# Kernel tuning notes

Measured on AMD Instinct MI355X. Metric: run time of the kernel, lower is better.

Reference implementation:

```python
import jax, jax.numpy as jnp
import numpy as np

OBS, ACT, LAT, H = 64, 32, 25, 5
B = 8192
SUP_H = 64


def setup_inputs() -> dict:
    key = jax.random.key(0)
    ks = jax.random.split(key, 12)
    s = 0.1
    inp = {
        'obs': jax.random.normal(ks[0], (B, OBS), jnp.float32),
        # supervisor FeedForward: OBS -> 64 -> 64 -> LAT, ReLU hidden, Sigmoid output
        'sw1': jax.random.normal(ks[1], (OBS, SUP_H), jnp.float32) * s,
        'sb1': jnp.zeros((SUP_H,), jnp.float32),
        'sw2': jax.random.normal(ks[2], (SUP_H, SUP_H), jnp.float32) * s,
        'sb2': jnp.zeros((SUP_H,), jnp.float32),
        'sw3': jax.random.normal(ks[3], (SUP_H, LAT), jnp.float32) * s,
        'sb3': jnp.zeros((LAT,), jnp.float32),
        # OBS*ACT tiny reflex FeedForwards 1 -> H -> 1, stacked into batched params
        'rw1': jax.random.normal(ks[4], (OBS, ACT, H), jnp.float32) * s,
        'rb1': jnp.zeros((OBS, ACT, H), jnp.float32),
        'rw2': jax.random.normal(ks[5], (OBS, ACT, H), jnp.float32) * s,
        'rb2': jnp.zeros((OBS, ACT), jnp.float32),
        # activation matrix (LAT, OBS, ACT)
        'act_matrix': jnp.ones((LAT, OBS, ACT), jnp.float32),
    }
    return inp


def reference(obs, sw1, sb1, sw2, sb2, sw3, sb3, rw1, rb1, rw2, rb2, act_matrix):
    # supervisor: (B, LAT) sigmoid latent activations
    h = jax.nn.relu(obs @ sw1 + sb1)
    h = jax.nn.relu(h @ sw2 + sb2)
    latent = jax.nn.sigmoid(h @ sw3 + sb3)

    # reflex gating: (B, LAT) x (LAT, OBS, ACT) -> (B, OBS, ACT), softmax over ACT
    logits = jnp.einsum('bl,loa->boa', latent, act_matrix)
    reflex_acts = jax.nn.softmax(logits, axis=-1)

    # all OBS*ACT tiny 1->H->1 MLPs, batched: input is obs[:, o] (scalar per net)
    # hidden: (B, OBS, ACT, H)
    rh = jax.nn.relu(obs[:, :, None, None] * rw1[None] + rb1[None])
    reflex_out = jnp.einsum('boah,oah->boa', rh, rw2) + rb2[None]  # (B, OBS, ACT)

    # weighted sum over obs dim -> (B, ACT)
    return jnp.sum(reflex_out * reflex_acts, axis=1)
```

## Files before the change

kernel.cpp:

```cpp
#include <hip/hip_runtime.h>


#define TOBS 64
#define TACT 32
#define TLAT 25
#define TB   8192
#define BT   16
#define NCH  16
#define HSTR 68

#define DPP_ADD(x, ctrl) \
  ((x) + __builtin_bit_cast(float, __builtin_amdgcn_update_dpp( \
      0, __builtin_bit_cast(int, (x)), (ctrl), 0xF, 0xF, true)))

__device__ __forceinline__ float halfwave_sum(float x) {
    x = DPP_ADD(x, 0xB1);
    x = DPP_ADD(x, 0x4E);
    x = DPP_ADD(x, 0x141);
    x = DPP_ADD(x, 0x140);
    int y = __builtin_amdgcn_ds_swizzle(__builtin_bit_cast(int, x), 0x401F);
    return x + __builtin_bit_cast(float, y);
}

__device__ __forceinline__ float sigmoidf_(float x) {
    return 1.0f / (1.0f + __expf(-x));
}

__global__ __launch_bounds__(256, 2)
void reflex_fused(const float* __restrict__ obs,
                  const float* __restrict__ sw1, const float* __restrict__ sb1,
                  const float* __restrict__ sw2, const float* __restrict__ sb2,
                  const float* __restrict__ sw3, const float* __restrict__ sb3,
                  const float* __restrict__ rw1, const float* __restrict__ rb1,
                  const float* __restrict__ rw2, const float* __restrict__ rb2,
                  const float* __restrict__ am,  float* __restrict__ out)
{
    __shared__ __align__(16) float obs_s[BT * HSTR];
    __shared__ __align__(16) float lat_s[BT * 26];
    __shared__ __align__(16) union {
        struct { float h1[BT * HSTR]; float h2[BT * HSTR]; } p1;
        struct { float4 At4[2][25 * 32]; float4 W4[2][16 * 32]; } p2;
    } U;

    const int tid  = threadIdx.x;
    const int row0 = blockIdx.x * BT;

    {
        const int r = tid >> 4, f = tid & 15;
        *(float4*)&obs_s[r * HSTR + f * 4] =
            *(const float4*)&obs[(row0 + r) * TOBS + f * 4];
    }
    __syncthreads();

    {
        const int r = tid >> 4, j0 = (tid & 15) * 4;
        float4 acc = *(const float4*)&sb1[j0];
        #pragma unroll 8
        for (int k = 0; k < 64; ++k) {
            float x = obs_s[r * HSTR + k];
            const float4 w = *(const float4*)&sw1[k * 64 + j0];
            acc.x = fmaf(x, w.x, acc.x); acc.y = fmaf(x, w.y, acc.y);
            acc.z = fmaf(x, w.z, acc.z); acc.w = fmaf(x, w.w, acc.w);
        }
        *(float4*)&U.p1.h1[r * HSTR + j0] =
            make_float4(fmaxf(acc.x, 0.f), fmaxf(acc.y, 0.f),
                        fmaxf(acc.z, 0.f), fmaxf(acc.w, 0.f));
    }
    __syncthreads();

    {
        const int r = tid >> 4, j0 = (tid & 15) * 4;
        float4 acc = *(const float4*)&sb2[j0];
        #pragma unroll 8
        for (int k = 0; k < 64; ++k) {
            float x = U.p1.h1[r * HSTR + k];
            const float4 w = *(const float4*)&sw2[k * 64 + j0];
            acc.x = fmaf(x, w.x, acc.x); acc.y = fmaf(x, w.y, acc.y);
            acc.z = fmaf(x, w.z, acc.z); acc.w = fmaf(x, w.w, acc.w);
        }
        *(float4*)&U.p1.h2[r * HSTR + j0] =
            make_float4(fmaxf(acc.x, 0.f), fmaxf(acc.y, 0.f),
                        fmaxf(acc.z, 0.f), fmaxf(acc.w, 0.f));
    }
    __syncthreads();

    {
        const int r = tid >> 4, q = tid & 15;
        if (q < 13) {
            const int j = q * 2;
            float a0 = sb3[j];
            float a1 = (j + 1 < TLAT) ? sb3[j + 1] : 0.f;
            #pragma unroll 8
            for (int k = 0; k < 64; ++k) {
                float x = U.p1.h2[r * HSTR + k];
                a0 = fmaf(x, sw3[k * TLAT + j], a0);
                if (j + 1 < TLAT) a1 = fmaf(x, sw3[k * TLAT + j + 1], a1);
            }
            lat_s[r * 26 + j] = sigmoidf_(a0);
            if (j + 1 < TLAT) lat_s[r * 26 + j + 1] = sigmoidf_(a1);
        }
    }
    __syncthreads();

    const int a  = tid & 31;
    const int hw = tid >> 5;
    const int r0 = hw * 2, r1 = r0 + 1;

    float latA[TLAT], latB[TLAT];
    #pragma unroll
    for (int l = 0; l < TLAT; ++l) {
        latA[l] = lat_s[r0 * 26 + l];
        latB[l] = lat_s[r1 * 26 + l];
    }

    auto wload = [&](int k, int n) -> float {
        if (k < 5)  return rw1[n * 5 + k];
        if (k < 10) return rb1[n * 5 + (k - 5)];
        if (k < 15) return rw2[n * 5 + (k - 10)];
        return rb2[n];
    };

    auto stage = [&](int c, int b) {
        const int cb = c * 128;
        {
            int e = tid, l = e >> 5, a_ = e & 31;
            const float* g = am + l * 2048 + cb + a_;
            float4 v; v.x = g[0]; v.y = g[32]; v.z = g[64]; v.w = g[96];
            U.p2.At4[b][e] = v;

            e = tid + 256; l = e >> 5; a_ = e & 31;
            const float* g2 = am + l * 2048 + cb + a_;
            float4 v2; v2.x = g2[0]; v2.y = g2[32]; v2.z = g2[64]; v2.w = g2[96];
            U.p2.At4[b][e] = v2;

            e = tid + 512; l = e >> 5; a_ = e & 31;
            const float* g3 = am + l * 2048 + cb + a_;
            float4 v3; v3.x = g3[0]; v3.y = g3[32]; v3.z = g3[64]; v3.w = g3[96];
            U.p2.At4[b][e] = v3;

            if (tid < 32) {
                e = tid + 768;
                const float* g4 = am + 24 * 2048 + cb + tid;
                float4 v4; v4.x = g4[0]; v4.y = g4[32]; v4.z = g4[64]; v4.w = g4[96];
                U.p2.At4[b][e] = v4;
            }
        }
        {
            int k = tid >> 5, a_ = tid & 31;
            int n0 = cb + a_;
            float4 w;
            w.x = wload(k, n0);      w.y = wload(k, n0 + 32);
            w.z = wload(k, n0 + 64); w.w = wload(k, n0 + 96);
            U.p2.W4[b][tid] = w;

            k += 8;
            float4 w2;
            w2.x = wload(k, n0);      w2.y = wload(k, n0 + 32);
            w2.z = wload(k, n0 + 64); w2.w = wload(k, n0 + 96);
            U.p2.W4[b][tid + 256] = w2;
        }
    };

    float acc0 = 0.f, acc1 = 0.f;

    stage(0, 0);
    __syncthreads();

    for (int c = 0; c < NCH; ++c) {
        const float4* A4 = U.p2.At4[c & 1];
        const float4* Wb = U.p2.W4[c & 1];

        float l00 = 0.f, l01 = 0.f, l02 = 0.f, l03 = 0.f;
        float l10 = 0.f, l11 = 0.f, l12 = 0.f, l13 = 0.f;
        #pragma unroll
        for (int l = 0; l < TLAT; ++l) {
            const float4 q = A4[l * 32 + a];
            l00 = fmaf(q.x, latA[l], l00); l10 = fmaf(q.x, latB[l], l10);
            l01 = fmaf(q.y, latA[l], l01); l11 = fmaf(q.y, latB[l], l11);
            l02 = fmaf(q.z, latA[l], l02); l12 = fmaf(q.z, latB[l], l12);
            l03 = fmaf(q.w, latA[l], l03); l13 = fmaf(q.w, latB[l], l13);
        }

        float e00 = __expf(l00), e01 = __expf(l01), e02 = __expf(l02), e03 = __expf(l03);
        float e10 = __expf(l10), e11 = __expf(l11), e12 = __expf(l12), e13 = __expf(l13);
        float p00 = e00 * __builtin_amdgcn_rcpf(halfwave_sum(e00));
        float p01 = e01 * __builtin_amdgcn_rcpf(halfwave_sum(e01));
        float p02 = e02 * __builtin_amdgcn_rcpf(halfwave_sum(e02));
        float p03 = e03 * __builtin_amdgcn_rcpf(halfwave_sum(e03));
        float p10 = e10 * __builtin_amdgcn_rcpf(halfwave_sum(e10));
        float p11 = e11 * __builtin_amdgcn_rcpf(halfwave_sum(e11));
        float p12 = e12 * __builtin_amdgcn_rcpf(halfwave_sum(e12));
        float p13 = e13 * __builtin_amdgcn_rcpf(halfwave_sum(e13));

        const int ob = c * 4;
        const float x00 = obs_s[r0 * HSTR + ob],     x10 = obs_s[r1 * HSTR + ob];
        const float x01 = obs_s[r0 * HSTR + ob + 1], x11 = obs_s[r1 * HSTR + ob + 1];
        const float x02 = obs_s[r0 * HSTR + ob + 2], x12 = obs_s[r1 * HSTR + ob + 2];
        const float x03 = obs_s[r0 * HSTR + ob + 3], x13 = obs_s[r1 * HSTR + ob + 3];

        const float4 B2 = Wb[15 * 32 + a];
        float q00 = B2.x, q01 = B2.y, q02 = B2.z, q03 = B2.w;
        float q10 = B2.x, q11 = B2.y, q12 = B2.z, q13 = B2.w;
        #pragma unroll
        for (int h = 0; h < 5; ++h) {
            const float4 w1v = Wb[h * 32 + a];
            const float4 b1v = Wb[(5 + h) * 32 + a];
            const float4 w2v = Wb[(10 + h) * 32 + a];
            q00 = fmaf(fmaxf(fmaf(x00, w1v.x, b1v.x), 0.f), w2v.x, q00);
            q10 = fmaf(fmaxf(fmaf(x10, w1v.x, b1v.x), 0.f), w2v.x, q10);
            q01 = fmaf(fmaxf(fmaf(x01, w1v.y, b1v.y), 0.f), w2v.y, q01);
            q11 = fmaf(fmaxf(fmaf(x11, w1v.y, b1v.y), 0.f), w2v.y, q11);
            q02 = fmaf(fmaxf(fmaf(x02, w1v.z, b1v.z), 0.f), w2v.z, q02);
            q12 = fmaf(fmaxf(fmaf(x12, w1v.z, b1v.z), 0.f), w2v.z, q12);
            q03 = fmaf(fmaxf(fmaf(x03, w1v.w, b1v.w), 0.f), w2v.w, q03);
            q13 = fmaf(fmaxf(fmaf(x13, w1v.w, b1v.w), 0.f), w2v.w, q13);
        }

        acc0 = fmaf(q00, p00, acc0); acc1 = fmaf(q10, p10, acc1);
        acc0 = fmaf(q01, p01, acc0); acc1 = fmaf(q11, p11, acc1);
        acc0 = fmaf(q02, p02, acc0); acc1 = fmaf(q12, p12, acc1);
        acc0 = fmaf(q03, p03, acc0); acc1 = fmaf(q13, p13, acc1);

        if (c + 1 < NCH) stage(c + 1, (c + 1) & 1);
        __syncthreads();
    }

    out[(row0 + r0) * TACT + a] = acc0;
    out[(row0 + r1) * TACT + a] = acc1;
}

extern "C" void kernel_launch(void* const* d_in, const int* in_sizes, int n_in,
                              void* d_out, int out_size, void* d_ws, size_t ws_size,
                              hipStream_t stream) {
    const float* obs = (const float*)d_in[0];
    const float* sw1 = (const float*)d_in[1];
    const float* sb1 = (const float*)d_in[2];
    const float* sw2 = (const float*)d_in[3];
    const float* sb2 = (const float*)d_in[4];
    const float* sw3 = (const float*)d_in[5];
    const float* sb3 = (const float*)d_in[6];
    const float* rw1 = (const float*)d_in[7];
    const float* rb1 = (const float*)d_in[8];
    const float* rw2 = (const float*)d_in[9];
    const float* rb2 = (const float*)d_in[10];
    const float* am  = (const float*)d_in[11];
    float* out = (float*)d_out;

    reflex_fused<<<TB / BT, 256, 0, stream>>>(obs, sw1, sb1, sw2, sb2, sw3, sb3,
                                              rw1, rb1, rw2, rb2, am, out);
}
```

Baseline: 57.97 us.

## Split obs dimension across block pairs and widen per-thread row tile to four

```diff
diff --git a/kernel.cpp b/kernel.cpp
--- a/kernel.cpp
+++ b/kernel.cpp
@@ -5,8 +5,8 @@
 #define TACT 32
 #define TLAT 25
 #define TB   8192
-#define BT   16
-#define NCH  16
+#define BT   32
+#define NCH  8
 #define HSTR 68
 
 #define DPP_ADD(x, ctrl) \
@@ -26,7 +26,7 @@
     return 1.0f / (1.0f + __expf(-x));
 }
 
-__global__ __launch_bounds__(256, 2)
+__global__ __launch_bounds__(256, 1)
 void reflex_fused(const float* __restrict__ obs,
                   const float* __restrict__ sw1, const float* __restrict__ sb1,
                   const float* __restrict__ sw2, const float* __restrict__ sb2,
@@ -42,76 +42,92 @@
         struct { float4 At4[2][25 * 32]; float4 W4[2][16 * 32]; } p2;
     } U;
 
-    const int tid  = threadIdx.x;
-    const int row0 = blockIdx.x * BT;
-
-    {
-        const int r = tid >> 4, f = tid & 15;
-        *(float4*)&obs_s[r * HSTR + f * 4] =
-            *(const float4*)&obs[(row0 + r) * TOBS + f * 4];
-    }
-    __syncthreads();
-
-    {
-        const int r = tid >> 4, j0 = (tid & 15) * 4;
-        float4 acc = *(const float4*)&sb1[j0];
-        #pragma unroll 8
-        for (int k = 0; k < 64; ++k) {
-            float x = obs_s[r * HSTR + k];
-            const float4 w = *(const float4*)&sw1[k * 64 + j0];
-            acc.x = fmaf(x, w.x, acc.x); acc.y = fmaf(x, w.y, acc.y);
-            acc.z = fmaf(x, w.z, acc.z); acc.w = fmaf(x, w.w, acc.w);
-        }
-        *(float4*)&U.p1.h1[r * HSTR + j0] =
-            make_float4(fmaxf(acc.x, 0.f), fmaxf(acc.y, 0.f),
-                        fmaxf(acc.z, 0.f), fmaxf(acc.w, 0.f));
-    }
-    __syncthreads();
-
-    {
-        const int r = tid >> 4, j0 = (tid & 15) * 4;
-        float4 acc = *(const float4*)&sb2[j0];
-        #pragma unroll 8
-        for (int k = 0; k < 64; ++k) {
-            float x = U.p1.h1[r * HSTR + k];
-            const float4 w = *(const float4*)&sw2[k * 64 + j0];
-            acc.x = fmaf(x, w.x, acc.x); acc.y = fmaf(x, w.y, acc.y);
-            acc.z = fmaf(x, w.z, acc.z); acc.w = fmaf(x, w.w, acc.w);
-        }
-        *(float4*)&U.p1.h2[r * HSTR + j0] =
-            make_float4(fmaxf(acc.x, 0.f), fmaxf(acc.y, 0.f),
-                        fmaxf(acc.z, 0.f), fmaxf(acc.w, 0.f));
-    }
-    __syncthreads();
-
-    {
-        const int r = tid >> 4, q = tid & 15;
+    const int tid   = threadIdx.x;
+    const int bid   = blockIdx.x;
+    const int row0  = (bid >> 1) * BT;
+    const int obase = (bid & 1) * 32;
+
+    {
+        const int r = tid >> 3, f = tid & 7;
+        *(float4*)&obs_s[r * HSTR + f * 8] =
+            *(const float4*)&obs[(row0 + r) * TOBS + f * 8];
+        *(float4*)&obs_s[r * HSTR + f * 8 + 4] =
+            *(const float4*)&obs[(row0 + r) * TOBS + f * 8 + 4];
+    }
+    __syncthreads();
+
+    {
+        const int rr = tid >> 4, j0 = (tid & 15) * 4;
+        #pragma unroll
+        for (int rp = 0; rp < BT; rp += 16) {
+            const int r = rp + rr;
+            float4 acc = *(const float4*)&sb1[j0];
+            #pragma unroll 8
+            for (int k = 0; k < 64; ++k) {
+                float x = obs_s[r * HSTR + k];
+                const float4 w = *(const float4*)&sw1[k * 64 + j0];
+                acc.x = fmaf(x, w.x, acc.x); acc.y = fmaf(x, w.y, acc.y);
+                acc.z = fmaf(x, w.z, acc.z); acc.w = fmaf(x, w.w, acc.w);
+            }
+            *(float4*)&U.p1.h1[r * HSTR + j0] =
+                make_float4(fmaxf(acc.x, 0.f), fmaxf(acc.y, 0.f),
+                            fmaxf(acc.z, 0.f), fmaxf(acc.w, 0.f));
+        }
+    }
+    __syncthreads();
+
+    {
+        const int rr = tid >> 4, j0 = (tid & 15) * 4;
+        #pragma unroll
+        for (int rp = 0; rp < BT; rp += 16) {
+            const int r = rp + rr;
+            float4 acc = *(const float4*)&sb2[j0];
+            #pragma unroll 8
+            for (int k = 0; k < 64; ++k) {
+                float x = U.p1.h1[r * HSTR + k];
+                const float4 w = *(const float4*)&sw2[k * 64 + j0];
+                acc.x = fmaf(x, w.x, acc.x); acc.y = fmaf(x, w.y, acc.y);
+                acc.z = fmaf(x, w.z, acc.z); acc.w = fmaf(x, w.w, acc.w);
+            }
+            *(float4*)&U.p1.h2[r * HSTR + j0] =
+                make_float4(fmaxf(acc.x, 0.f), fmaxf(acc.y, 0.f),
+                            fmaxf(acc.z, 0.f), fmaxf(acc.w, 0.f));
+        }
+    }
+    __syncthreads();
+
+    {
+        const int rr = tid >> 4, q = tid & 15;
         if (q < 13) {
             const int j = q * 2;
-            float a0 = sb3[j];
-            float a1 = (j + 1 < TLAT) ? sb3[j + 1] : 0.f;
-            #pragma unroll 8
-            for (int k = 0; k < 64; ++k) {
-                float x = U.p1.h2[r * HSTR + k];
-                a0 = fmaf(x, sw3[k * TLAT + j], a0);
-                if (j + 1 < TLAT) a1 = fmaf(x, sw3[k * TLAT + j + 1], a1);
-            }
-            lat_s[r * 26 + j] = sigmoidf_(a0);
-            if (j + 1 < TLAT) lat_s[r * 26 + j + 1] = sigmoidf_(a1);
+            #pragma unroll
+            for (int rp = 0; rp < BT; rp += 16) {
+                const int r = rp + rr;
+                float a0 = sb3[j];
+                float a1 = (j + 1 < TLAT) ? sb3[j + 1] : 0.f;
+                #pragma unroll 8
+                for (int k = 0; k < 64; ++k) {
+                    float x = U.p1.h2[r * HSTR + k];
+                    a0 = fmaf(x, sw3[k * TLAT + j], a0);
+                    if (j + 1 < TLAT) a1 = fmaf(x, sw3[k * TLAT + j + 1], a1);
+                }
+                lat_s[r * 26 + j] = sigmoidf_(a0);
+                if (j + 1 < TLAT) lat_s[r * 26 + j + 1] = sigmoidf_(a1);
+            }
         }
     }
     __syncthreads();
 
     const int a  = tid & 31;
-    const int hw = tid >> 5;
-    const int r0 = hw * 2, r1 = r0 + 1;
-
-    float latA[TLAT], latB[TLAT];
+    const int g  = tid >> 5;
+    const int r0 = g * 4;
+
+    float lat[4][25];
     #pragma unroll
-    for (int l = 0; l < TLAT; ++l) {
-        latA[l] = lat_s[r0 * 26 + l];
-        latB[l] = lat_s[r1 * 26 + l];
-    }
+    for (int rr = 0; rr < 4; ++rr)
+        #pragma unroll
+        for (int l = 0; l < TLAT; ++l)
+            lat[rr][l] = lat_s[(r0 + rr) * 26 + l];
 
     auto wload = [&](int k, int n) -> float {
         if (k < 5)  return rw1[n * 5 + k];
@@ -121,11 +137,11 @@
     };
 
     auto stage = [&](int c, int b) {
-        const int cb = c * 128;
+        const int cb = obase * 32 + c * 128;
         {
             int e = tid, l = e >> 5, a_ = e & 31;
-            const float* g = am + l * 2048 + cb + a_;
-            float4 v; v.x = g[0]; v.y = g[32]; v.z = g[64]; v.w = g[96];
+            const float* gp = am + l * 2048 + cb + a_;
+            float4 v; v.x = gp[0]; v.y = gp[32]; v.z = gp[64]; v.w = gp[96];
             U.p2.At4[b][e] = v;
 
             e = tid + 256; l = e >> 5; a_ = e & 31;
@@ -139,10 +155,9 @@
             U.p2.At4[b][e] = v3;
 
             if (tid < 32) {
-                e = tid + 768;
                 const float* g4 = am + 24 * 2048 + cb + tid;
                 float4 v4; v4.x = g4[0]; v4.y = g4[32]; v4.z = g4[64]; v4.w = g4[96];
-                U.p2.At4[b][e] = v4;
+                U.p2.At4[b][tid + 768] = v4;
             }
         }
         {
@@ -161,7 +176,7 @@
         }
     };
 
-    float acc0 = 0.f, acc1 = 0.f;
+    float acc[4] = {0.f, 0.f, 0.f, 0.f};
 
     stage(0, 0);
     __syncthreads();
@@ -170,63 +185,80 @@
         const float4* A4 = U.p2.At4[c & 1];
         const float4* Wb = U.p2.W4[c & 1];
 
-        float l00 = 0.f, l01 = 0.f, l02 = 0.f, l03 = 0.f;
-        float l10 = 0.f, l11 = 0.f, l12 = 0.f, l13 = 0.f;
+        float lg[4][4] = {{0.f,0.f,0.f,0.f},{0.f,0.f,0.f,0.f},
+                          {0.f,0.f,0.f,0.f},{0.f,0.f,0.f,0.f}};
         #pragma unroll
         for (int l = 0; l < TLAT; ++l) {
             const float4 q = A4[l * 32 + a];
-            l00 = fmaf(q.x, latA[l], l00); l10 = fmaf(q.x, latB[l], l10);
-            l01 = fmaf(q.y, latA[l], l01); l11 = fmaf(q.y, latB[l], l11);
-            l02 = fmaf(q.z, latA[l], l02); l12 = fmaf(q.z, latB[l], l12);
-            l03 = fmaf(q.w, latA[l], l03); l13 = fmaf(q.w, latB[l], l13);
-        }
-
-        float e00 = __expf(l00), e01 = __expf(l01), e02 = __expf(l02), e03 = __expf(l03);
-        float e10 = __expf(l10), e11 = __expf(l11), e12 = __expf(l12), e13 = __expf(l13);
-        float p00 = e00 * __builtin_amdgcn_rcpf(halfwave_sum(e00));
-        float p01 = e01 * __builtin_amdgcn_rcpf(halfwave_sum(e01));
-        float p02 = e02 * __builtin_amdgcn_rcpf(halfwave_sum(e02));
-        float p03 = e03 * __builtin_amdgcn_rcpf(halfwave_sum(e03));
-        float p10 = e10 * __builtin_amdgcn_rcpf(halfwave_sum(e10));
-        float p11 = e11 * __builtin_amdgcn_rcpf(halfwave_sum(e11));
-        float p12 = e12 * __builtin_amdgcn_rcpf(halfwave_sum(e12));
-        float p13 = e13 * __builtin_amdgcn_rcpf(halfwave_sum(e13));
-
-        const int ob = c * 4;
-        const float x00 = obs_s[r0 * HSTR + ob],     x10 = obs_s[r1 * HSTR + ob];
-        const float x01 = obs_s[r0 * HSTR + ob + 1], x11 = obs_s[r1 * HSTR + ob + 1];
-        const float x02 = obs_s[r0 * HSTR + ob + 2], x12 = obs_s[r1 * HSTR + ob + 2];
-        const float x03 = obs_s[r0 * HSTR + ob + 3], x13 = obs_s[r1 * HSTR + ob + 3];
+            #pragma unroll
+            for (int rr = 0; rr < 4; ++rr) {
+                lg[rr][0] = fmaf(q.x, lat[rr][l], lg[rr][0]);
+                lg[rr][1] = fmaf(q.y, lat[rr][l], lg[rr][1]);
+                lg[rr][2] = fmaf(q.z, lat[rr][l], lg[rr][2]);
+                lg[rr][3] = fmaf(q.w, lat[rr][l], lg[rr][3]);
+            }
+        }
+
+        float p[4][4];
+        #pragma unroll
+        for (int rr = 0; rr < 4; ++rr) {
+            #pragma unroll
+            for (int oo = 0; oo < 4; ++oo) {
+                float e = __expf(lg[rr][oo]);
+                p[rr][oo] = e * __builtin_amdgcn_rcpf(halfwave_sum(e));
+            }
+        }
+
+        const int ob = obase + c * 4;
+        float4 xv0 = *(const float4*)&obs_s[(r0 + 0) * HSTR + ob];
+        float4 xv1 = *(const float4*)&obs_s[(r0 + 1) * HSTR + ob];
+        float4 xv2 = *(const float4*)&obs_s[(r0 + 2) * HSTR + ob];
+        float4 xv3 = *(const float4*)&obs_s[(r0 + 3) * HSTR + ob];
 
         const float4 B2 = Wb[15 * 32 + a];
-        float q00 = B2.x, q01 = B2.y, q02 = B2.z, q03 = B2.w;
-        float q10 = B2.x, q11 = B2.y, q12 = B2.z, q13 = B2.w;
+        float q_[4][4];
+        #pragma unroll
+        for (int rr = 0; rr < 4; ++rr) {
+            q_[rr][0] = B2.x; q_[rr][1] = B2.y; q_[rr][2] = B2.z; q_[rr][3] = B2.w;
+        }
         #pragma unroll
         for (int h = 0; h < 5; ++h) {
             const float4 w1v = Wb[h * 32 + a];
             const float4 b1v = Wb[(5 + h) * 32 + a];
             const float4 w2v = Wb[(10 + h) * 32 + a];
-            q00 = fmaf(fmaxf(fmaf(x00, w1v.x, b1v.x), 0.f), w2v.x, q00);
-            q10 = fmaf(fmaxf(fmaf(x10, w1v.x, b1v.x), 0.f), w2v.x, q10);
-            q01 = fmaf(fmaxf(fmaf(x01, w1v.y, b1v.y), 0.f), w2v.y, q01);
-            q11 = fmaf(fmaxf(fmaf(x11, w1v.y, b1v.y), 0.f), w2v.y, q11);
-            q02 = fmaf(fmaxf(fmaf(x02, w1v.z, b1v.z), 0.f), w2v.z, q02);
-            q12 = fmaf(fmaxf(fmaf(x12, w1v.z, b1v.z), 0.f), w2v.z, q12);
-            q03 = fmaf(fmaxf(fmaf(x03, w1v.w, b1v.w), 0.f), w2v.w, q03);
-            q13 = fmaf(fmaxf(fmaf(x13, w1v.w, b1v.w), 0.f), w2v.w, q13);
-        }
-
-        acc0 = fmaf(q00, p00, acc0); acc1 = fmaf(q10, p10, acc1);
-        acc0 = fmaf(q01, p01, acc0); acc1 = fmaf(q11, p11, acc1);
-        acc0 = fmaf(q02, p02, acc0); acc1 = fmaf(q12, p12, acc1);
-        acc0 = fmaf(q03, p03, acc0); acc1 = fmaf(q13, p13, acc1);
+            q_[0][0] = fmaf(fmaxf(fmaf(xv0.x, w1v.x, b1v.x), 0.f), w2v.x, q_[0][0]);
+            q_[0][1] = fmaf(fmaxf(fmaf(xv0.y, w1v.y, b1v.y), 0.f), w2v.y, q_[0][1]);
+            q_[0][2] = fmaf(fmaxf(fmaf(xv0.z, w1v.z, b1v.z), 0.f), w2v.z, q_[0][2]);
+            q_[0][3] = fmaf(fmaxf(fmaf(xv0.w, w1v.w, b1v.w), 0.f), w2v.w, q_[0][3]);
+            q_[1][0] = fmaf(fmaxf(fmaf(xv1.x, w1v.x, b1v.x), 0.f), w2v.x, q_[1][0]);
+            q_[1][1] = fmaf(fmaxf(fmaf(xv1.y, w1v.y, b1v.y), 0.f), w2v.y, q_[1][1]);
+            q_[1][2] = fmaf(fmaxf(fmaf(xv1.z, w1v.z, b1v.z), 0.f), w2v.z, q_[1][2]);
+            q_[1][3] = fmaf(fmaxf(fmaf(xv1.w, w1v.w, b1v.w), 0.f), w2v.w, q_[1][3]);
+            q_[2][0] = fmaf(fmaxf(fmaf(xv2.x, w1v.x, b1v.x), 0.f), w2v.x, q_[2][0]);
+            q_[2][1] = fmaf(fmaxf(fmaf(xv2.y, w1v.y, b1v.y), 0.f), w2v.y, q_[2][1]);
+            q_[2][2] = fmaf(fmaxf(fmaf(xv2.z, w1v.z, b1v.z), 0.f), w2v.z, q_[2][2]);
+            q_[2][3] = fmaf(fmaxf(fmaf(xv2.w, w1v.w, b1v.w), 0.f), w2v.w, q_[2][3]);
+            q_[3][0] = fmaf(fmaxf(fmaf(xv3.x, w1v.x, b1v.x), 0.f), w2v.x, q_[3][0]);
+            q_[3][1] = fmaf(fmaxf(fmaf(xv3.y, w1v.y, b1v.y), 0.f), w2v.y, q_[3][1]);
+            q_[3][2] = fmaf(fmaxf(fmaf(xv3.z, w1v.z, b1v.z), 0.f), w2v.z, q_[3][2]);
+            q_[3][3] = fmaf(fmaxf(fmaf(xv3.w, w1v.w, b1v.w), 0.f), w2v.w, q_[3][3]);
+        }
+
+        #pragma unroll
+        for (int rr = 0; rr < 4; ++rr) {
+            acc[rr] = fmaf(q_[rr][0], p[rr][0], acc[rr]);
+            acc[rr] = fmaf(q_[rr][1], p[rr][1], acc[rr]);
+            acc[rr] = fmaf(q_[rr][2], p[rr][2], acc[rr]);
+            acc[rr] = fmaf(q_[rr][3], p[rr][3], acc[rr]);
+        }
 
         if (c + 1 < NCH) stage(c + 1, (c + 1) & 1);
         __syncthreads();
     }
 
-    out[(row0 + r0) * TACT + a] = acc0;
-    out[(row0 + r1) * TACT + a] = acc1;
+    #pragma unroll
+    for (int rr = 0; rr < 4; ++rr)
+        unsafeAtomicAdd(&out[(row0 + r0 + rr) * TACT + a], acc[rr]);
 }
 
 extern "C" void kernel_launch(void* const* d_in, const int* in_sizes, int n_in,
@@ -246,6 +278,7 @@
     const float* am  = (const float*)d_in[11];
     float* out = (float*)d_out;
 
-    reflex_fused<<<TB / BT, 256, 0, stream>>>(obs, sw1, sb1, sw2, sb2, sw3, sb3,
-                                              rw1, rb1, rw2, rb2, am, out);
-}
+    hipMemsetAsync(out, 0, (size_t)out_size * sizeof(float), stream);
+    reflex_fused<<<(TB / BT) * 2, 256, 0, stream>>>(obs, sw1, sb1, sw2, sb2, sw3, sb3,
+                                                    rw1, rb1, rw2, rb2, am, out);
+}
```

New measurement: 92.26 us. +59.2%, slower.
